# Kernel optimization log

Measured on AMD Instinct MI355X. Metric: run time of the kernel, lower is better.

The kernel has to match this reference:

```python
import jax, jax.numpy as jnp
import numpy as np
import math

B = 65536
N_NUM = 64; N_CAT = 16; CAT_SIZE = 1000; EMB = 16
ND = 64; NA = 64; OUT = ND + NA; NSTEPS = 5; GAMMA = 1.5
NFEAT = N_NUM + N_CAT * EMB          # 320
NGROUPS = N_NUM + N_CAT              # 80
GROUP_IDX = np.repeat(np.arange(NGROUPS), [1] * N_NUM + [EMB] * N_CAT)  # len 320
RES_SCALE = math.sqrt(0.5)
BN_EPS = 1e-5


def setup_inputs() -> dict:
    keys = iter(jax.random.split(jax.random.key(0), 64))
    def rn(shape, std):
        return jax.random.normal(next(keys), shape, jnp.float32) * std
    def mk_bn(c, lead=()):
        # stacked (scale, bias, running_mean, running_var) along axis -2
        s = 1.0 + 0.05 * jax.random.normal(next(keys), (*lead, c), jnp.float32)
        b = 0.05 * jax.random.normal(next(keys), (*lead, c), jnp.float32)
        m = 0.05 * jax.random.normal(next(keys), (*lead, c), jnp.float32)
        v = 1.0 + 0.1 * jax.random.uniform(next(keys), (*lead, c), dtype=jnp.float32)
        return jnp.stack([s, b, m, v], axis=-2)
    inp = {}
    inp["x_num"] = jax.random.normal(next(keys), (B, N_NUM), jnp.float32)
    inp["x_cat"] = jax.random.randint(next(keys), (B, N_CAT), 0, CAT_SIZE)
    inp["emb_W"] = rn((N_CAT, CAT_SIZE, EMB), 0.1)
    inp["in_bn"] = mk_bn(NFEAT)
    inp["sh_W0"] = rn((NFEAT, 2 * OUT), 1.0 / math.sqrt(NFEAT))
    inp["sh_b0"] = jnp.zeros((2 * OUT,), jnp.float32)
    inp["sh_bn0"] = mk_bn(2 * OUT)
    inp["sh_W1"] = rn((OUT, 2 * OUT), 1.0 / math.sqrt(OUT))
    inp["sh_b1"] = jnp.zeros((2 * OUT,), jnp.float32)
    inp["sh_bn1"] = mk_bn(2 * OUT)
    inp["init_W"] = rn((2, OUT, 2 * OUT), 1.0 / math.sqrt(OUT))
    inp["init_b"] = jnp.zeros((2, 2 * OUT), jnp.float32)
    inp["init_bn"] = mk_bn(2 * OUT, (2,))
    inp["step_W"] = rn((NSTEPS, 2, OUT, 2 * OUT), 1.0 / math.sqrt(OUT))
    inp["step_b"] = jnp.zeros((NSTEPS, 2, 2 * OUT), jnp.float32)
    inp["step_bn"] = mk_bn(2 * OUT, (NSTEPS, 2))
    inp["att_W"] = rn((NSTEPS, NA, NGROUPS), 1.0 / math.sqrt(NA))
    inp["att_b"] = jnp.zeros((NSTEPS, NGROUPS), jnp.float32)
    inp["att_bn"] = mk_bn(NGROUPS, (NSTEPS,))
    inp["out_W"] = rn((ND, 1), 1.0 / math.sqrt(ND))
    inp["out_b"] = jnp.zeros((1,), jnp.float32)
    return inp


def bn_apply(x, p):
    s, b, m, v = p  # each [C]
    return (x - m) * jax.lax.rsqrt(v + BN_EPS) * s + b


def glu_layer(x, W, b, bn):
    h = bn_apply(x @ W + b, bn)          # [B, 2*OUT]
    o, g = jnp.split(h, 2, axis=1)
    return o * jax.nn.sigmoid(g)


def glu_block(x, W, b, bn):
    y = glu_layer(x, W, b, bn)
    return (x + y) * RES_SCALE if x.shape == y.shape else y


def sparsemax(z):
    # along axis=1; Martins & Astudillo 2016
    zs = -jnp.sort(-z, axis=1)
    cs = jnp.cumsum(zs, axis=1)
    r = jnp.arange(1, z.shape[1] + 1, dtype=z.dtype)
    support = (1.0 + r * zs) > cs
    k = jnp.maximum(support.sum(axis=1, keepdims=True), 1)
    cs_k = jnp.take_along_axis(cs, k - 1, axis=1)
    tau = (cs_k - 1.0) / k.astype(z.dtype)
    return jnp.maximum(z - tau, 0.0)


def _forward(x_num, x_cat, emb_W, in_bn, sh_W0, sh_b0, sh_bn0, sh_W1, sh_b1, sh_bn1,
             init_W, init_b, init_bn, step_W, step_b, step_bn, att_W, att_b, att_bn,
             out_W, out_b):
    # categorical embeddings: [B, N_CAT, EMB] -> [B, N_CAT*EMB]
    emb = emb_W[np.arange(N_CAT)[None, :], x_cat].reshape(x_cat.shape[0], -1)
    x = jnp.concatenate([x_num, emb], axis=1)  # [B, NFEAT]
    x = bn_apply(x, in_bn)

    def ft_shared(h):
        h = glu_block(h, sh_W0, sh_b0, sh_bn0)   # 320 -> 128, no residual
        return glu_block(h, sh_W1, sh_b1, sh_bn1)  # residual

    def ft_indep(h, W, b, bn):
        for i in range(W.shape[0]):
            h = glu_block(h, W[i], b[i], bn[i])
        return h

    out0 = ft_indep(ft_shared(x), init_W, init_b, init_bn)
    a = out0[:, ND:]
    prior = jnp.ones((x.shape[0], NGROUPS), x.dtype)
    decision_sum = jnp.zeros((x.shape[0], ND), x.dtype)
    for step in range(NSTEPS):
        logits = bn_apply(a @ att_W[step] + att_b[step], att_bn[step]) * prior
        mask_group = sparsemax(logits)           # [B, NGROUPS]
        prior = prior * (GAMMA - mask_group)
        mask = mask_group[:, GROUP_IDX]          # [B, NFEAT] (repeat_interleave)
        out = ft_indep(ft_shared(mask * x), step_W[step], step_b[step], step_bn[step])
        d, a = out[:, :ND], out[:, ND:]
        decision_sum = decision_sum + jax.nn.relu(d)
    return decision_sum @ out_W + out_b          # [B, 1]


def reference(x_num, x_cat, emb_W, in_bn, sh_W0, sh_b0, sh_bn0, sh_W1, sh_b1, sh_bn1,
              init_W, init_b, init_bn, step_W, step_b, step_bn, att_W, att_b, att_bn,
              out_W, out_b):
    return _forward(x_num, x_cat, emb_W, in_bn, sh_W0, sh_b0, sh_bn0, sh_W1, sh_b1,
                    sh_bn1, init_W, init_b, init_bn, step_W, step_b, step_bn,
                    att_W, att_b, att_bn, out_W, out_b)
```

## Files before the change

### kernel.cpp

```cpp
#include <hip/hip_runtime.h>
#include <math.h>
#include <stdint.h>

typedef _Float16 half_t;
typedef _Float16 half8 __attribute__((ext_vector_type(8)));
typedef float floatx4 __attribute__((ext_vector_type(4)));
typedef float floatx16 __attribute__((ext_vector_type(16)));

constexpr float BN_EPS_C = 1e-5f;
constexpr float RES_SCALE_C = 0.70710678118654752f;
constexpr float GAMMA_C = 1.5f;
#define B_TOT 65536

__device__ __forceinline__ uint32_t pack2(float y) {
    const half_t h = (half_t)y;
    const half_t l = (half_t)(y - (float)h);
    union { half_t f; unsigned short u; } a, b; a.f = h; b.f = l;
    return (uint32_t)a.u | ((uint32_t)b.u << 16);
}
__device__ __forceinline__ void unpack2(uint32_t v, half_t& h, half_t& l) {
    union { unsigned short u; half_t f; } a, b;
    a.u = (unsigned short)(v & 0xffffu); b.u = (unsigned short)(v >> 16);
    h = a.f; l = b.f;
}

__global__ void wsplit_kernel(const float* __restrict__ sh_W0, const float* __restrict__ sh_W1,
                              const float* __restrict__ init_W, const float* __restrict__ step_W,
                              half_t* __restrict__ Wh, half_t* __restrict__ Wl)
{
    const int b = blockIdx.x, n = threadIdx.x;
    const float* src; int k; size_t base;
    if (b < 320)      { src = sh_W0;           k = b;       base = 0; }
    else if (b < 448) { src = sh_W1;           k = b - 320; base = 81920; }
    else if (b < 576) { src = init_W;          k = b - 448; base = 114688; }
    else if (b < 704) { src = init_W + 32768;  k = b - 576; base = 147456; }
    else {
        int j = (b - 704) >> 7; k = (b - 704) & 127;
        src = step_W + (size_t)j * 32768; base = 180224 + (size_t)j * 32768;
    }
    const float v = src[k * 256 + n];
    const half_t hi = (half_t)v;
    const half_t lo = (half_t)(v - (float)hi);
    const size_t idx = base + (size_t)(((k >> 3) * 256 + n) * 8 + (k & 7));
    Wh[idx] = hi; Wl[idx] = lo;
}

__global__ void wsplit_att_kernel(const float* __restrict__ att_W,
                                  half_t* __restrict__ aWh, half_t* __restrict__ aWl)
{
    const int b = blockIdx.x;
    const int n = threadIdx.x;
    const int step = b >> 6, k = b & 63;
    const float v = att_W[(size_t)b * 80 + n];
    const half_t h = (half_t)v;
    const half_t l = (half_t)(v - (float)h);
    const size_t idx = (size_t)step * 5120 + (size_t)(((k >> 3) * 80 + n) * 8 + (k & 7));
    aWh[idx] = h; aWl[idx] = l;
}

__global__ void embed_bn_kernel(const float* __restrict__ x_num, const int* __restrict__ x_cat,
                                const float* __restrict__ emb_W, const float* __restrict__ in_bn,
                                uint32_t* __restrict__ xp)
{
    const int idx = blockIdx.x * 256 + threadIdx.x;
    const int s = idx / 320, j = idx - s * 320;
    float v;
    if (j < 64) v = x_num[(size_t)s * 64 + j];
    else {
        const int c = (j - 64) >> 4, e = (j - 64) & 15;
        v = emb_W[(size_t)(c * 1000 + x_cat[(size_t)s * 16 + c]) * 16 + e];
    }
    const float val = (v - in_bn[640 + j]) * (in_bn[j] * __frsqrt_rn(in_bn[960 + j] + BN_EPS_C)) + in_bn[320 + j];
    xp[idx] = pack2(val);
}

__device__ __forceinline__ void bn_fold(const float* __restrict__ bn, const float* __restrict__ bias,
                                        int c, float& sc, float& sh)
{
    sc = bn[c] * __frsqrt_rn(bn[768 + c] + BN_EPS_C);
    sh = fmaf(bias[c] - bn[512 + c], sc, bn[256 + c]);
}

__device__ __forceinline__ float glu_val(float accO, float accG,
                                         float sc_o, float sh_o, float sc_g, float sh_g)
{
    const float o = fmaf(accO, sc_o, sh_o);
    const float g = fmaf(accG, sc_g, sh_g);
    const float e = __expf(-g);
    return o * __builtin_amdgcn_rcpf(1.f + e);
}

#define MFMA32(A, B, C) C = __builtin_amdgcn_mfma_f32_32x32x16_f16(A, B, C, 0, 0, 0)
#define MFMA16(A, B, C) C = __builtin_amdgcn_mfma_f32_16x16x32_f16(A, B, C, 0, 0, 0)

__device__ __forceinline__ void layer_accum(const half_t (*H_h)[136], const half_t (*H_l)[136],
                                            const half_t* __restrict__ Wh, const half_t* __restrict__ Wl,
                                            size_t off, int n32, int k8, int no, int rot,
                                            floatx16* accO, floatx16* accG)
{
#pragma unroll 1
    for (int s = 0; s < 8; ++s) {
        const int sl8 = (s + rot) & 7;
        const int kq = sl8 * 2 + k8;
        const size_t wo = off + (size_t)(kq * 256 + no + n32) * 8;
        const half8 bo_h = *(const half8*)(Wh + wo);
        const half8 bo_l = *(const half8*)(Wl + wo);
        const half8 bg_h = *(const half8*)(Wh + wo + 1024);
        const half8 bg_l = *(const half8*)(Wl + wo + 1024);
#pragma unroll
        for (int mt = 0; mt < 4; ++mt) {
            const half8 a_h = *(const half8*)&H_h[mt * 32 + n32][sl8 * 16 + k8 * 8];
            const half8 a_l = *(const half8*)&H_l[mt * 32 + n32][sl8 * 16 + k8 * 8];
            MFMA32(a_h, bo_h, accO[mt]); MFMA32(a_h, bg_h, accG[mt]);
            MFMA32(a_l, bo_h, accO[mt]); MFMA32(a_l, bg_h, accG[mt]);
            MFMA32(a_h, bo_l, accO[mt]); MFMA32(a_h, bg_l, accG[mt]);
        }
    }
}

template<bool MASK>
__global__ __launch_bounds__(256, 2)
void ft_chain(const uint32_t* __restrict__ xp, uint32_t* __restrict__ avp,
              const half_t* __restrict__ Wh, const half_t* __restrict__ Wl,
              const half_t* __restrict__ aWh, const half_t* __restrict__ aWl,
              const float* __restrict__ att_b, const float* __restrict__ att_bn,
              float* __restrict__ prior,
              const float* __restrict__ b1, const float* __restrict__ bn1,
              const float* __restrict__ b2, const float* __restrict__ bn2,
              const float* __restrict__ b3, const float* __restrict__ bn3,
              const float* __restrict__ b4, const float* __restrict__ bn4,
              size_t w3_off, size_t w4_off,
              float* __restrict__ ds, int wmode_last, int step)
{
    __shared__ __align__(16) char smem[79872];
    float    (*mgs)[84]  = (float    (*)[84])smem;
    half_t   (*As_h)[72] = (half_t   (*)[72])(smem + 43008);
    half_t   (*As_l)[72] = (half_t   (*)[72])(smem + 61440);
    uint32_t (*Apk)[68]  = (uint32_t (*)[68])(smem + 43008);
    half_t   (*H_h)[136] = (half_t   (*)[136])smem;
    half_t   (*H_l)[136] = (half_t   (*)[136])(smem + 34816);

    const int t = threadIdx.x;
    const int s0 = blockIdx.x * 128;
    const int w = t >> 6, lane = t & 63;
    const int n32 = lane & 31, k8 = lane >> 5;
    const int quad = lane >> 4, l16 = lane & 15;
    const int no = 32 * w;
    const int half_id = (blockIdx.x >> 8) & 1;
    const int row = t >> 1, k0 = (t & 1) * 32;

    if (MASK) {
        {
            const uint4* src = (const uint4*)(avp + (size_t)(s0 + row) * 64 + k0);
            uint4* dst = (uint4*)&Apk[row][k0];
#pragma unroll
            for (int q = 0; q < 8; ++q) dst[q] = src[q];
        }
        __syncthreads();
        floatx4 zacc[2][5];
#pragma unroll
        for (int mt = 0; mt < 2; ++mt)
#pragma unroll
            for (int nt = 0; nt < 5; ++nt) zacc[mt][nt] = (floatx4){0.f, 0.f, 0.f, 0.f};
#pragma unroll
        for (int kc = 0; kc < 64; kc += 32) {
            half8 a_h[2], a_l[2];
#pragma unroll
            for (int mt = 0; mt < 2; ++mt) {
                uint32_t wv[8];
                *(uint4*)&wv[0] = *(const uint4*)&Apk[w * 32 + mt * 16 + l16][kc + quad * 8];
                *(uint4*)&wv[4] = *(const uint4*)&Apk[w * 32 + mt * 16 + l16][kc + quad * 8 + 4];
#pragma unroll
                for (int j = 0; j < 8; ++j) { half_t h, l; unpack2(wv[j], h, l); a_h[mt][j] = h; a_l[mt][j] = l; }
            }
            const int kq = (kc >> 3) + quad;
#pragma unroll
            for (int nt = 0; nt < 5; ++nt) {
                const size_t wi = (size_t)(kq * 80 + nt * 16 + l16) * 8;
                const half8 b_h = *(const half8*)(aWh + wi);
                const half8 b_l = *(const half8*)(aWl + wi);
#pragma unroll
                for (int mt = 0; mt < 2; ++mt) {
                    MFMA16(a_h[mt], b_h, zacc[mt][nt]);
                    MFMA16(a_l[mt], b_h, zacc[mt][nt]);
                    MFMA16(a_h[mt], b_l, zacc[mt][nt]);
                }
            }
        }
        float preg[2][5][4];
#pragma unroll
        for (int nt = 0; nt < 5; ++nt) {
            const int c = nt * 16 + l16;
            const float sc = att_bn[c] * __frsqrt_rn(att_bn[240 + c] + BN_EPS_C);
            const float sh = fmaf(att_b[c] - att_bn[160 + c], sc, att_bn[80 + c]);
#pragma unroll
            for (int mt = 0; mt < 2; ++mt)
#pragma unroll
                for (int r = 0; r < 4; ++r) {
                    const int sl = w * 32 + mt * 16 + quad * 4 + r;
                    const float pr = (step == 0) ? 1.f : prior[(size_t)(s0 + sl) * 80 + c];
                    preg[mt][nt][r] = pr;
                    mgs[sl][c] = fmaf(zacc[mt][nt][r], sc, sh) * pr;
                }
        }
        __syncthreads();
        {
            const int samp = row, j0 = (t & 1) * 40;
            float zj[40], zmax = -1e30f;
#pragma unroll
            for (int j = 0; j < 40; ++j) { zj[j] = mgs[samp][j0 + j]; zmax = fmaxf(zmax, zj[j]); }
            zmax = fmaxf(zmax, __shfl_xor(zmax, 1));
            float lo = zmax - 1.f, hi = zmax;
#pragma unroll 1
            for (int it = 0; it < 22; ++it) {
                const float mid = 0.5f * (lo + hi);
                float ssum = 0.f;
#pragma unroll
                for (int j = 0; j < 40; ++j) ssum += fmaxf(zj[j] - mid, 0.f);
                ssum += __shfl_xor(ssum, 1);
                if (ssum >= 1.f) lo = mid; else hi = mid;
            }
            const float tau = 0.5f * (lo + hi);
#pragma unroll
            for (int j = 0; j < 40; ++j) mgs[samp][j0 + j] = fmaxf(zj[j] - tau, 0.f);
        }
        __syncthreads();
#pragma unroll
        for (int nt = 0; nt < 5; ++nt) {
            const int c = nt * 16 + l16;
#pragma unroll
            for (int mt = 0; mt < 2; ++mt)
#pragma unroll
                for (int r = 0; r < 4; ++r) {
                    const int sl = w * 32 + mt * 16 + quad * 4 + r;
                    prior[(size_t)(s0 + sl) * 80 + c] = preg[mt][nt][r] * (GAMMA_C - mgs[sl][c]);
                }
        }
    }

    floatx16 accO[4], accG[4];
#pragma unroll
    for (int i = 0; i < 4; ++i) { accO[i] = (floatx16)(0.f); accG[i] = (floatx16)(0.f); }

    const uint32_t* arow = xp + (size_t)(s0 + row) * 320 + k0;
    uint32_t pfw[32];
    int ic = half_id * 2;
#pragma unroll
    for (int q = 0; q < 8; ++q)
        *(uint4*)&pfw[q * 4] = *(const uint4*)(arow + ic * 64 + q * 4);

#pragma unroll 1
    for (int i = 0; i < 5; ++i) {
        __syncthreads();
        {
            const int kb = ic * 64 + k0;
            float mA = 1.f, mB = 1.f;
            if (MASK && ic != 0) {
                mA = mgs[row][64 + ((kb - 64) >> 4)];
                mB = mgs[row][64 + ((kb - 48) >> 4)];
            }
#pragma unroll
            for (int q = 0; q < 4; ++q) {
                half8 hh, ll;
                if (MASK && ic == 0) {
                    const float4 m0q = *(const float4*)&mgs[row][kb + q * 8];
                    const float4 m1q = *(const float4*)&mgs[row][kb + q * 8 + 4];
                    const float mm[8] = {m0q.x, m0q.y, m0q.z, m0q.w, m1q.x, m1q.y, m1q.z, m1q.w};
#pragma unroll
                    for (int j = 0; j < 8; ++j) {
                        half_t h, l; unpack2(pfw[q * 8 + j], h, l);
                        const float v = ((float)h + (float)l) * mm[j];
                        const half_t nh = (half_t)v;
                        hh[j] = nh; ll[j] = (half_t)(v - (float)nh);
                    }
                } else if (MASK) {
                    const float m = (q < 2) ? mA : mB;
#pragma unroll
                    for (int j = 0; j < 8; ++j) {
                        half_t h, l; unpack2(pfw[q * 8 + j], h, l);
                        const float v = ((float)h + (float)l) * m;
                        const half_t nh = (half_t)v;
                        hh[j] = nh; ll[j] = (half_t)(v - (float)nh);
                    }
                } else {
#pragma unroll
                    for (int j = 0; j < 8; ++j) { half_t h, l; unpack2(pfw[q * 8 + j], h, l); hh[j] = h; ll[j] = l; }
                }
                *(half8*)&As_h[row][k0 + q * 8] = hh;
                *(half8*)&As_l[row][k0 + q * 8] = ll;
            }
        }
        __syncthreads();
        const int icn = (ic + 1 == 5) ? 0 : ic + 1;
        if (i < 4) {
#pragma unroll
            for (int q = 0; q < 8; ++q)
                *(uint4*)&pfw[q * 4] = *(const uint4*)(arow + icn * 64 + q * 4);
        }
#pragma unroll
        for (int sl4 = 0; sl4 < 4; ++sl4) {
            const int kq = ic * 8 + sl4 * 2 + k8;
            const size_t wo = (size_t)(kq * 256 + no + n32) * 8;
            const half8 bo_h = *(const half8*)(Wh + wo);
            const half8 bo_l = *(const half8*)(Wl + wo);
            const half8 bg_h = *(const half8*)(Wh + wo + 1024);
            const half8 bg_l = *(const half8*)(Wl + wo + 1024);
#pragma unroll
            for (int mt = 0; mt < 4; ++mt) {
                const half8 a_h = *(const half8*)&As_h[mt * 32 + n32][sl4 * 16 + k8 * 8];
                const half8 a_l = *(const half8*)&As_l[mt * 32 + n32][sl4 * 16 + k8 * 8];
                MFMA32(a_h, bo_h, accO[mt]); MFMA32(a_h, bg_h, accG[mt]);
                MFMA32(a_l, bo_h, accO[mt]); MFMA32(a_l, bg_h, accG[mt]);
                MFMA32(a_h, bo_l, accO[mt]); MFMA32(a_h, bg_l, accG[mt]);
            }
        }
        ic = icn;
    }
    __syncthreads();

    {
        const int c = no + n32;
        float sc_o, sh_o, sc_g, sh_g;
        bn_fold(bn1, b1, c, sc_o, sh_o);
        bn_fold(bn1, b1, c + 128, sc_g, sh_g);
#pragma unroll
        for (int mt = 0; mt < 4; ++mt)
#pragma unroll
            for (int reg = 0; reg < 16; ++reg) {
                const int sl = mt * 32 + (reg & 3) + 8 * (reg >> 2) + 4 * k8;
                const float y = glu_val(accO[mt][reg], accG[mt][reg], sc_o, sh_o, sc_g, sh_g);
                const half_t nh = (half_t)y;
                H_h[sl][c] = nh; H_l[sl][c] = (half_t)(y - (float)nh);
            }
    }
    __syncthreads();

#pragma unroll 1
    for (int layer = 0; layer < 2; ++layer) {
        const float* bb = layer ? b3 : b2;
        const float* bn = layer ? bn3 : bn2;
        const size_t off = layer ? w3_off : (size_t)81920;
#pragma unroll
        for (int i = 0; i < 4; ++i) { accO[i] = (floatx16)(0.f); accG[i] = (floatx16)(0.f); }
        layer_accum(H_h, H_l, Wh, Wl, off, n32, k8, no, half_id * 4, accO, accG);
        __syncthreads();
        {
            const int c = no + n32;
            float sc_o, sh_o, sc_g, sh_g;
            bn_fold(bn, bb, c, sc_o, sh_o);
            bn_fold(bn, bb, c + 128, sc_g, sh_g);
#pragma unroll
            for (int mt = 0; mt < 4; ++mt)
#pragma unroll
                for (int reg = 0; reg < 16; ++reg) {
                    const int sl = mt * 32 + (reg & 3) + 8 * (reg >> 2) + 4 * k8;
                    const float res = (float)H_h[sl][c] + (float)H_l[sl][c];
                    const float y = (glu_val(accO[mt][reg], accG[mt][reg], sc_o, sh_o, sc_g, sh_g) + res) * RES_SCALE_C;
                    const half_t nh = (half_t)y;
                    H_h[sl][c] = nh; H_l[sl][c] = (half_t)(y - (float)nh);
                }
        }
        __syncthreads();
    }

#pragma unroll
    for (int i = 0; i < 4; ++i) { accO[i] = (floatx16)(0.f); accG[i] = (floatx16)(0.f); }
    layer_accum(H_h, H_l, Wh, Wl, w4_off, n32, k8, no, half_id * 4, accO, accG);
    {
        const int c = no + n32;
        float sc_o, sh_o, sc_g, sh_g;
        bn_fold(bn4, b4, c, sc_o, sh_o);
        bn_fold(bn4, b4, c + 128, sc_g, sh_g);
        if (w < 2) {
            if (wmode_last != 1) {
#pragma unroll
                for (int mt = 0; mt < 4; ++mt)
#pragma unroll
                    for (int reg = 0; reg < 16; ++reg) {
                        const int sl = mt * 32 + (reg & 3) + 8 * (reg >> 2) + 4 * k8;
                        const float res = (float)H_h[sl][c] + (float)H_l[sl][c];
                        const float y = (glu_val(accO[mt][reg], accG[mt][reg], sc_o, sh_o, sc_g, sh_g) + res) * RES_SCALE_C;
                        const float d = fmaxf(y, 0.f);
                        float* dp = ds + (size_t)(s0 + sl) * 64 + c;
                        *dp = (wmode_last == 2) ? d : (*dp + d);
                    }
            }
        } else {
#pragma unroll
            for (int mt = 0; mt < 4; ++mt)
#pragma unroll
                for (int reg = 0; reg < 16; ++reg) {
                    const int sl = mt * 32 + (reg & 3) + 8 * (reg >> 2) + 4 * k8;
                    const float res = (float)H_h[sl][c] + (float)H_l[sl][c];
                    const float y = (glu_val(accO[mt][reg], accG[mt][reg], sc_o, sh_o, sc_g, sh_g) + res) * RES_SCALE_C;
                    avp[(size_t)(s0 + sl) * 64 + (c - 64)] = pack2(y);
                }
        }
    }
}

__global__ void final_kernel(const float* __restrict__ dsum, const float* __restrict__ out_W,
                             const float* __restrict__ out_b, float* __restrict__ out)
{
    const int s = blockIdx.x * 256 + threadIdx.x;
    float acc = out_b[0];
    const float4* dp = (const float4*)(dsum + (size_t)s * 64);
    const float4* wp = (const float4*)out_W;
#pragma unroll
    for (int q = 0; q < 16; ++q) {
        const float4 d = dp[q];
        const float4 ww = wp[q];
        acc += d.x * ww.x + d.y * ww.y + d.z * ww.z + d.w * ww.w;
    }
    out[s] = acc;
}

extern "C" void kernel_launch(void* const* d_in, const int* in_sizes, int n_in,
                              void* d_out, int out_size, void* d_ws, size_t ws_size,
                              hipStream_t stream)
{
    const float* x_num  = (const float*)d_in[0];
    const int*   x_cat  = (const int*)d_in[1];
    const float* emb_W  = (const float*)d_in[2];
    const float* in_bn  = (const float*)d_in[3];
    const float* sh_W0  = (const float*)d_in[4];
    const float* sh_b0  = (const float*)d_in[5];
    const float* sh_bn0 = (const float*)d_in[6];
    const float* sh_W1  = (const float*)d_in[7];
    const float* sh_b1  = (const float*)d_in[8];
    const float* sh_bn1 = (const float*)d_in[9];
    const float* init_W = (const float*)d_in[10];
    const float* init_b = (const float*)d_in[11];
    const float* init_bn= (const float*)d_in[12];
    const float* step_W = (const float*)d_in[13];
    const float* step_b = (const float*)d_in[14];
    const float* step_bn= (const float*)d_in[15];
    const float* att_W  = (const float*)d_in[16];
    const float* att_b  = (const float*)d_in[17];
    const float* att_bn = (const float*)d_in[18];
    const float* out_W  = (const float*)d_in[19];
    const float* out_b  = (const float*)d_in[20];

    const size_t B = B_TOT;
    char* p = (char*)d_ws;
    uint32_t* xp  = (uint32_t*)p;  p += B * 320 * 4;
    uint32_t* avp = (uint32_t*)p;  p += B * 64 * 4;
    half_t* Wh    = (half_t*)p;    p += 507904 * 2;
    half_t* Wl    = (half_t*)p;    p += 507904 * 2;
    half_t* aWh   = (half_t*)p;    p += 25600 * 2;
    half_t* aWl   = (half_t*)p;    p += 25600 * 2;
    float* pri    = (float*)p;     p += B * 80 * 4;
    float* ds     = (float*)p;     p += B * 64 * 4;

    wsplit_kernel<<<1984, 256, 0, stream>>>(sh_W0, sh_W1, init_W, step_W, Wh, Wl);
    wsplit_att_kernel<<<320, 80, 0, stream>>>(att_W, aWh, aWl);
    embed_bn_kernel<<<(B_TOT * 320) / 256, 256, 0, stream>>>(x_num, x_cat, emb_W, in_bn, xp);

    const int GB = B_TOT / 128;
    ft_chain<false><<<GB, 256, 0, stream>>>(xp, avp, Wh, Wl,
                                            nullptr, nullptr, nullptr, nullptr, nullptr,
                                            sh_b0, sh_bn0, sh_b1, sh_bn1,
                                            init_b, init_bn, init_b + 256, init_bn + 1024,
                                            (size_t)114688, (size_t)147456, ds, 1, 0);
    for (int st = 0; st < 5; ++st) {
        const size_t w3 = 180224 + (size_t)(st * 2 + 0) * 32768;
        const size_t w4 = 180224 + (size_t)(st * 2 + 1) * 32768;
        ft_chain<true><<<GB, 256, 0, stream>>>(xp, avp, Wh, Wl,
                                               aWh + st * 5120, aWl + st * 5120,
                                               att_b + st * 80, att_bn + st * 320, pri,
                                               sh_b0, sh_bn0, sh_b1, sh_bn1,
                                               step_b + (st * 2 + 0) * 256, step_bn + (st * 2 + 0) * 1024,
                                               step_b + (st * 2 + 1) * 256, step_bn + (st * 2 + 1) * 1024,
                                               w3, w4, ds, st == 0 ? 2 : 3, st);
    }
    final_kernel<<<B_TOT / 256, 256, 0, stream>>>(ds, out_W, out_b, (float*)d_out);
}
```

Baseline: 778.5 us.

## Use packed fp16 conversion in GLU epilogues, unroll K loop, trim sparsemax bisection

Replaces the per-element fp32-to-fp16 hi/lo split in the GLU epilogues with packed round-toward-zero conversions (cvt_pkrtz) that handle two values per instruction. It also unrolls the MFMA K-slice loop by two to expose more load/MFMA overlap, and cuts the sparsemax threshold bisection from 22 to 16 iterations. Round-toward-zero changes rounding of the hi part, though the lo residual compensates. Fewer bisection steps loosen the sparsemax threshold accuracy, and the extra unroll may raise register pressure.

```diff
diff --git a/kernel.cpp b/kernel.cpp
--- a/kernel.cpp
+++ b/kernel.cpp
@@ -4,6 +4,7 @@
 
 typedef _Float16 half_t;
 typedef _Float16 half8 __attribute__((ext_vector_type(8)));
+typedef __fp16 fp16x2 __attribute__((ext_vector_type(2)));
 typedef float floatx4 __attribute__((ext_vector_type(4)));
 typedef float floatx16 __attribute__((ext_vector_type(16)));
 
@@ -22,6 +23,19 @@
     union { unsigned short u; half_t f; } a, b;
     a.u = (unsigned short)(v & 0xffffu); b.u = (unsigned short)(v >> 16);
     h = a.f; l = b.f;
+}
+__device__ __forceinline__ void split_pair(float y0, float y1, half_t& h0, half_t& l0, half_t& h1, half_t& l1) {
+    fp16x2 hh = __builtin_amdgcn_cvt_pkrtz(y0, y1);
+    fp16x2 ll = __builtin_amdgcn_cvt_pkrtz(y0 - (float)hh.x, y1 - (float)hh.y);
+    h0 = (half_t)hh.x; l0 = (half_t)ll.x; h1 = (half_t)hh.y; l1 = (half_t)ll.y;
+}
+__device__ __forceinline__ void pack2_pair(float y0, float y1, uint32_t& w0, uint32_t& w1) {
+    fp16x2 hh = __builtin_amdgcn_cvt_pkrtz(y0, y1);
+    fp16x2 ll = __builtin_amdgcn_cvt_pkrtz(y0 - (float)hh.x, y1 - (float)hh.y);
+    const uint32_t hb = __builtin_bit_cast(uint32_t, hh);
+    const uint32_t lb = __builtin_bit_cast(uint32_t, ll);
+    w0 = (hb & 0xffffu) | (lb << 16);
+    w1 = (hb >> 16) | (lb & 0xffff0000u);
 }
 
 __global__ void wsplit_kernel(const float* __restrict__ sh_W0, const float* __restrict__ sh_W1,
@@ -98,7 +112,7 @@
                                             size_t off, int n32, int k8, int no, int rot,
                                             floatx16* accO, floatx16* accG)
 {
-#pragma unroll 1
+#pragma unroll 2
     for (int s = 0; s < 8; ++s) {
         const int sl8 = (s + rot) & 7;
         const int kq = sl8 * 2 + k8;
@@ -212,7 +226,7 @@
             zmax = fmaxf(zmax, __shfl_xor(zmax, 1));
             float lo = zmax - 1.f, hi = zmax;
 #pragma unroll 1
-            for (int it = 0; it < 22; ++it) {
+            for (int it = 0; it < 16; ++it) {
                 const float mid = 0.5f * (lo + hi);
                 float ssum = 0.f;
 #pragma unroll
@@ -326,12 +340,18 @@
 #pragma unroll
         for (int mt = 0; mt < 4; ++mt)
 #pragma unroll
-            for (int reg = 0; reg < 16; ++reg) {
-                const int sl = mt * 32 + (reg & 3) + 8 * (reg >> 2) + 4 * k8;
-                const float y = glu_val(accO[mt][reg], accG[mt][reg], sc_o, sh_o, sc_g, sh_g);
-                const half_t nh = (half_t)y;
-                H_h[sl][c] = nh; H_l[sl][c] = (half_t)(y - (float)nh);
-            }
+            for (int q = 0; q < 4; ++q)
+#pragma unroll
+                for (int rp = 0; rp < 2; ++rp) {
+                    const int r0 = q * 4 + rp * 2;
+                    const int sl = mt * 32 + rp * 2 + 8 * q + 4 * k8;
+                    const float y0 = glu_val(accO[mt][r0],     accG[mt][r0],     sc_o, sh_o, sc_g, sh_g);
+                    const float y1 = glu_val(accO[mt][r0 + 1], accG[mt][r0 + 1], sc_o, sh_o, sc_g, sh_g);
+                    half_t h0, l0, h1, l1;
+                    split_pair(y0, y1, h0, l0, h1, l1);
+                    H_h[sl][c] = h0; H_l[sl][c] = l0;
+                    H_h[sl + 1][c] = h1; H_l[sl + 1][c] = l1;
+                }
     }
     __syncthreads();
 
@@ -352,13 +372,20 @@
 #pragma unroll
             for (int mt = 0; mt < 4; ++mt)
 #pragma unroll
-                for (int reg = 0; reg < 16; ++reg) {
-                    const int sl = mt * 32 + (reg & 3) + 8 * (reg >> 2) + 4 * k8;
-                    const float res = (float)H_h[sl][c] + (float)H_l[sl][c];
-                    const float y = (glu_val(accO[mt][reg], accG[mt][reg], sc_o, sh_o, sc_g, sh_g) + res) * RES_SCALE_C;
-                    const half_t nh = (half_t)y;
-                    H_h[sl][c] = nh; H_l[sl][c] = (half_t)(y - (float)nh);
-                }
+                for (int q = 0; q < 4; ++q)
+#pragma unroll
+                    for (int rp = 0; rp < 2; ++rp) {
+                        const int r0 = q * 4 + rp * 2;
+                        const int sl = mt * 32 + rp * 2 + 8 * q + 4 * k8;
+                        const float res0 = (float)H_h[sl][c] + (float)H_l[sl][c];
+                        const float res1 = (float)H_h[sl + 1][c] + (float)H_l[sl + 1][c];
+                        const float y0 = (glu_val(accO[mt][r0],     accG[mt][r0],     sc_o, sh_o, sc_g, sh_g) + res0) * RES_SCALE_C;
+                        const float y1 = (glu_val(accO[mt][r0 + 1], accG[mt][r0 + 1], sc_o, sh_o, sc_g, sh_g) + res1) * RES_SCALE_C;
+                        half_t h0, l0, h1, l1;
+                        split_pair(y0, y1, h0, l0, h1, l1);
+                        H_h[sl][c] = h0; H_l[sl][c] = l0;
+                        H_h[sl + 1][c] = h1; H_l[sl + 1][c] = l1;
+                    }
         }
         __syncthreads();
     }
@@ -389,12 +416,20 @@
 #pragma unroll
             for (int mt = 0; mt < 4; ++mt)
 #pragma unroll
-                for (int reg = 0; reg < 16; ++reg) {
-                    const int sl = mt * 32 + (reg & 3) + 8 * (reg >> 2) + 4 * k8;
-                    const float res = (float)H_h[sl][c] + (float)H_l[sl][c];
-                    const float y = (glu_val(accO[mt][reg], accG[mt][reg], sc_o, sh_o, sc_g, sh_g) + res) * RES_SCALE_C;
-                    avp[(size_t)(s0 + sl) * 64 + (c - 64)] = pack2(y);
-                }
+                for (int q = 0; q < 4; ++q)
+#pragma unroll
+                    for (int rp = 0; rp < 2; ++rp) {
+                        const int r0 = q * 4 + rp * 2;
+                        const int sl = mt * 32 + rp * 2 + 8 * q + 4 * k8;
+                        const float res0 = (float)H_h[sl][c] + (float)H_l[sl][c];
+                        const float res1 = (float)H_h[sl + 1][c] + (float)H_l[sl + 1][c];
+                        const float y0 = (glu_val(accO[mt][r0],     accG[mt][r0],     sc_o, sh_o, sc_g, sh_g) + res0) * RES_SCALE_C;
+                        const float y1 = (glu_val(accO[mt][r0 + 1], accG[mt][r0 + 1], sc_o, sh_o, sc_g, sh_g) + res1) * RES_SCALE_C;
+                        uint32_t w0, w1;
+                        pack2_pair(y0, y1, w0, w1);
+                        avp[(size_t)(s0 + sl) * 64 + (c - 64)] = w0;
+                        avp[(size_t)(s0 + sl + 1) * 64 + (c - 64)] = w1;
+                    }
         }
     }
 }
```

Measured after the change: 781.6 us. Within noise of the previous version (+0.4%).
